# Optimization experiments

Hardware: AMD Instinct MI355X
Metric: run time of the kernel (lower is better)

## Reference

```python
import jax, jax.numpy as jnp
import numpy as np

B, L, LO, H, V = 8, 1024, 1024, 768, 4096
NUM_TAGS = 256


def _merge_one(tags):
    """Replicates merge_weights() for one sequence of tags [L].

    A maximal run of equal, non-(-1) tags becomes one output row that averages
    the hidden states over the run. A run is only emitted when it is *closed*
    by a tag change or a -1 (so a run ending at the last position is dropped,
    exactly like the torch loop). Remaining rows are zero with bias -100.
    """
    Ls = tags.shape[0]
    pos = jnp.arange(Ls)
    valid = tags != -1
    prev = jnp.concatenate([jnp.full((1,), -2, tags.dtype), tags[:-1]])
    start = valid & ((pos == 0) | (tags != prev) | (prev == -1))
    seg_id = jnp.cumsum(start.astype(jnp.int32)) - 1          # run index per position
    total_runs = seg_id[-1] + 1
    emitted = total_runs - valid[-1].astype(jnp.int32)        # trailing open run dropped
    seg_clip = jnp.clip(seg_id, 0, Ls - 1)
    # run lengths via segment sum (invalid positions contribute 0)
    counts = jax.ops.segment_sum(valid.astype(jnp.float32), seg_clip, num_segments=Ls)
    w = jnp.where(valid & (seg_id >= 0) & (seg_id < emitted),
                  1.0 / jnp.maximum(counts[seg_clip], 1.0), 0.0)
    merge = jnp.zeros((Ls, Ls), jnp.float32).at[seg_clip, pos].add(w)  # [rows, tokens]
    bias = jnp.where(pos < emitted, 0.0, -100.0)
    return merge, bias


def setup_inputs() -> dict:
    key = jax.random.key(0)
    k1, k2, k3, k4 = jax.random.split(key, 4)
    hidden1_states = jax.random.normal(k1, (B, L, H), jnp.float32)
    hidden2_states = jax.random.normal(k2, (B, LO, H), jnp.float32)
    lm_logits = jax.random.normal(k3, (B, LO, V), jnp.float32)
    tags = jnp.sort(jax.random.randint(k4, (B, L), 0, NUM_TAGS), axis=-1)
    return {"hidden1_states": hidden1_states, "hidden2_states": hidden2_states,
            "lm_logits": lm_logits, "tags": tags}


def reference(hidden1_states, hidden2_states, lm_logits, tags):
    merge, bias = jax.vmap(_merge_one)(tags)                     # [B,L,L], [B,L]
    attn = jnp.einsum('bls,bsh->blh', merge, hidden1_states)     # segment means
    attn1 = jnp.einsum('boh,blh->bol', hidden2_states, attn) + bias[:, None, :]
    return jnp.concatenate([lm_logits, attn1], axis=2)           # [B,LO,V+L]
```

## Files before the change

### kernel.cpp

```cpp
#include <hip/hip_runtime.h>
#include <hip/hip_bf16.h>
#include <stdint.h>

#define BB   8
#define LL   1024
#define LOO  1024
#define HH   768
#define VV   4096
#define OUTW 5120
#define EMAX 256

typedef unsigned short ushort_t;
typedef __attribute__((ext_vector_type(4))) float   f32x4;
typedef __attribute__((ext_vector_type(8))) __bf16  bf16x8;
typedef __attribute__((ext_vector_type(4))) float   float4v;
typedef __attribute__((ext_vector_type(4))) int     int4v;
typedef __attribute__((ext_vector_type(4))) unsigned short ushort4v;

static __device__ __forceinline__ ushort_t f2bf(float f) {
    union { float f; uint32_t u; } v; v.f = f;
    uint32_t u = v.u;
    uint32_t r = (u + 0x7fffu + ((u >> 16) & 1u)) >> 16;
    return (ushort_t)r;
}

__global__ __launch_bounds__(256) void attn_fused_kernel(
        const float* __restrict__ h1,
        const int* __restrict__ tags,
        ushort_t* __restrict__ attn,
        int* __restrict__ emitted_out) {
    int b = blockIdx.x >> 8;
    int r = blockIdx.x & 255;
    int tid = threadIdx.x;

    __shared__ int stags[LL];
    __shared__ int cnt[256];
    __shared__ int runpos[EMAX + 2];

    ((int4v*)stags)[tid] = ((const int4v*)(tags + b * LL))[tid];
    __syncthreads();

    int p0 = tid * 4;
    int st[4];
    int prevm1 = (p0 == 0) ? -2 : stags[p0 - 1];
    st[0] = (p0 == 0) || (stags[p0] != prevm1);
    st[1] = (stags[p0 + 1] != stags[p0]);
    st[2] = (stags[p0 + 2] != stags[p0 + 1]);
    st[3] = (stags[p0 + 3] != stags[p0 + 2]);
    int c = st[0] + st[1] + st[2] + st[3];
    cnt[tid] = c;
    __syncthreads();
    for (int off = 1; off < 256; off <<= 1) {
        int v = cnt[tid];
        int a = (tid >= off) ? cnt[tid - off] : 0;
        __syncthreads();
        cnt[tid] = v + a;
        __syncthreads();
    }
    int total = cnt[255];
    int base = cnt[tid] - c;
#pragma unroll
    for (int j = 0; j < 4; ++j)
        if (st[j]) runpos[base++] = p0 + j;
    if (tid == 0) runpos[total] = LL;
    __syncthreads();

    int em = total - 1;
    if (r == 0 && tid == 0) emitted_out[b] = em;

    ushort_t* arow = attn + ((size_t)b * EMAX + r) * HH;
    if (r >= em) {
        arow[tid] = 0; arow[tid + 256] = 0; arow[tid + 512] = 0;
        return;
    }
    int s = runpos[r], e = runpos[r + 1];
    float inv = 1.0f / (float)(e - s);
    const float* hb = h1 + (size_t)b * LL * HH;
    float a0 = 0.f, a1 = 0.f, a2 = 0.f;
    for (int p = s; p < e; ++p) {
        const float* row = hb + (size_t)p * HH;
        a0 += row[tid]; a1 += row[tid + 256]; a2 += row[tid + 512];
    }
    arow[tid]       = f2bf(a0 * inv);
    arow[tid + 256] = f2bf(a1 * inv);
    arow[tid + 512] = f2bf(a2 * inv);
}

__global__ __launch_bounds__(256, 4) void fused_out_kernel(
        const float* __restrict__ h2,
        const ushort_t* __restrict__ Bm,
        const int* __restrict__ emitted,
        const float* __restrict__ lm,
        float* __restrict__ out) {
    __shared__ char smem[34816];

    const int bid = blockIdx.x;
    const int b   = bid >> 6;
    const int r0  = (bid & 63) << 4;

    const int tid  = threadIdx.x;
    const int lane = tid & 63;
    const int w    = tid >> 6;

    const float*    Ab = h2 + ((size_t)b * LOO + r0) * HH;
    const ushort_t* Bb = Bm + (size_t)b * EMAX * HH;

    f32x4 zero = {0.f, 0.f, 0.f, 0.f};
    f32x4 acc[4];
    acc[0] = zero; acc[1] = zero; acc[2] = zero; acc[3] = zero;

    const int arow_s = tid >> 4;
    const int akq    = tid & 15;
    for (int k0 = 0; k0 < HH; k0 += 64) {
        __syncthreads();
        {
            f32x4 v = *(const f32x4*)(Ab + (size_t)arow_s * HH + k0 + akq * 4);
            ushort4v o;
            o[0] = f2bf(v[0]); o[1] = f2bf(v[1]); o[2] = f2bf(v[2]); o[3] = f2bf(v[3]);
            *(ushort4v*)(smem + arow_s * 128 + ((akq * 8) ^ ((arow_s & 7) << 4))) = o;
        }
#pragma unroll
        for (int i = 0; i < 8; ++i) {
            int off = i * 4096 + tid * 16;
            int row = off >> 7;
            int cb  = off & 127;
            int scb = cb ^ ((row & 7) << 4);
            const ushort_t* gb = Bb + (size_t)row * HH + k0 + (scb >> 1);
            __builtin_amdgcn_global_load_lds(
                (const __attribute__((address_space(1))) void*)gb,
                (__attribute__((address_space(3))) void*)(smem + 2048 + off), 16, 0, 0);
        }
        asm volatile("s_waitcnt vmcnt(0)" ::: "memory");
        __syncthreads();

#pragma unroll
        for (int ks = 0; ks < 2; ++ks) {
            int kb   = (ks << 6) + ((lane >> 4) << 4);
            int ar   = lane & 15;
            bf16x8 af = *(const bf16x8*)(smem + ar * 128 + (kb ^ ((ar & 7) << 4)));
#pragma unroll
            for (int ni = 0; ni < 4; ++ni) {
                int br = ((w << 2) + ni) * 16 + (lane & 15);
                bf16x8 bf = *(const bf16x8*)(smem + 2048 + br * 128 + (kb ^ ((br & 7) << 4)));
                acc[ni] = __builtin_amdgcn_mfma_f32_16x16x32_bf16(af, bf, acc[ni], 0, 0, 0);
            }
        }
    }

    {
        int em = emitted[b];
        float* outb = out + ((size_t)b * LOO + r0) * OUTW + VV;
#pragma unroll
        for (int ni = 0; ni < 4; ++ni) {
            int l = ((w << 2) + ni) * 16 + (lane & 15);
            float badd = (l < em) ? 0.0f : -100.0f;
            int rbase = (lane >> 4) << 2;
#pragma unroll
            for (int rr = 0; rr < 4; ++rr)
                outb[(size_t)(rbase + rr) * OUTW + l] = acc[ni][rr] + badd;
        }
    }

    const float4v* lm4 = (const float4v*)lm + ((size_t)b * LOO + r0) * (VV / 4);
    float4v* o4 = (float4v*)out + ((size_t)b * LOO + r0) * (OUTW / 4);
    float4v fv = {-100.f, -100.f, -100.f, -100.f};
#pragma unroll 2
    for (int r = 0; r < 16; ++r) {
        float4v v0 = __builtin_nontemporal_load(&lm4[r * 1024 + tid]);
        float4v v1 = __builtin_nontemporal_load(&lm4[r * 1024 + tid + 256]);
        float4v v2 = __builtin_nontemporal_load(&lm4[r * 1024 + tid + 512]);
        float4v v3 = __builtin_nontemporal_load(&lm4[r * 1024 + tid + 768]);
        __builtin_nontemporal_store(v0, &o4[r * 1280 + tid]);
        __builtin_nontemporal_store(v1, &o4[r * 1280 + tid + 256]);
        __builtin_nontemporal_store(v2, &o4[r * 1280 + tid + 512]);
        __builtin_nontemporal_store(v3, &o4[r * 1280 + tid + 768]);
        if (tid < 192)
            __builtin_nontemporal_store(fv, &o4[r * 1280 + 1088 + tid]);
    }
}

extern "C" void kernel_launch(void* const* d_in, const int* in_sizes, int n_in,
                              void* d_out, int out_size, void* d_ws, size_t ws_size,
                              hipStream_t stream) {
    const float* h1   = (const float*)d_in[0];
    const float* h2   = (const float*)d_in[1];
    const float* lm   = (const float*)d_in[2];
    const int*   tags = (const int*)d_in[3];
    float* out = (float*)d_out;

    char* ws = (char*)d_ws;
    ushort_t* attn    = (ushort_t*)ws;
    int*      emitted = (int*)(ws + 3145728);

    attn_fused_kernel<<<BB * EMAX, 256, 0, stream>>>(h1, tags, attn, emitted);
    fused_out_kernel<<<512, 256, 0, stream>>>(h2, attn, emitted, lm, out);
}
```

Measured before the change: 86.32 us.

## Restructure segment-mean into position-chunk blocks and split GEMM from logits copy

The segment-mean kernel now assigns each block a 64-position chunk and a 256-column slice, locating the runs in that chunk by binary search and striding over columns per thread, so h1 is read more contiguously by fewer blocks. The output kernel is split into 64 larger GEMM blocks (128x256 tiles, 512 threads, register-prefetched double staging with padded LDS rows) and 1024 separate copy blocks for the lm_logits passthrough and the -100 fill. This aims to improve B-operand reuse and let the memory-bound copy run alongside the GEMM. The trade-off is that only 64 GEMM blocks exist, which may underuse the CUs, and the padded-stride LDS layout may introduce bank conflicts.

```diff
diff --git a/kernel.cpp b/kernel.cpp
--- a/kernel.cpp
+++ b/kernel.cpp
@@ -13,9 +13,9 @@
 typedef unsigned short ushort_t;
 typedef __attribute__((ext_vector_type(4))) float   f32x4;
 typedef __attribute__((ext_vector_type(8))) __bf16  bf16x8;
+typedef __attribute__((ext_vector_type(4))) __bf16  bf16x4;
 typedef __attribute__((ext_vector_type(4))) float   float4v;
 typedef __attribute__((ext_vector_type(4))) int     int4v;
-typedef __attribute__((ext_vector_type(4))) unsigned short ushort4v;
 
 static __device__ __forceinline__ ushort_t f2bf(float f) {
     union { float f; uint32_t u; } v; v.f = f;
@@ -24,18 +24,19 @@
     return (ushort_t)r;
 }
 
-__global__ __launch_bounds__(256) void attn_fused_kernel(
+__global__ __launch_bounds__(256) void attn_stream_kernel(
         const float* __restrict__ h1,
         const int* __restrict__ tags,
         ushort_t* __restrict__ attn,
         int* __restrict__ emitted_out) {
-    int b = blockIdx.x >> 8;
-    int r = blockIdx.x & 255;
-    int tid = threadIdx.x;
+    const int rc  = blockIdx.x;
+    const int cc  = blockIdx.y;
+    const int b   = blockIdx.z;
+    const int tid = threadIdx.x;
 
     __shared__ int stags[LL];
     __shared__ int cnt[256];
-    __shared__ int runpos[EMAX + 2];
+    __shared__ int runpos[EMAX + 1];
 
     ((int4v*)stags)[tid] = ((const int4v*)(tags + b * LL))[tid];
     __syncthreads();
@@ -47,8 +48,8 @@
     st[1] = (stags[p0 + 1] != stags[p0]);
     st[2] = (stags[p0 + 2] != stags[p0 + 1]);
     st[3] = (stags[p0 + 3] != stags[p0 + 2]);
-    int c = st[0] + st[1] + st[2] + st[3];
-    cnt[tid] = c;
+    int c4 = st[0] + st[1] + st[2] + st[3];
+    cnt[tid] = c4;
     __syncthreads();
     for (int off = 1; off < 256; off <<= 1) {
         int v = cnt[tid];
@@ -58,7 +59,7 @@
         __syncthreads();
     }
     int total = cnt[255];
-    int base = cnt[tid] - c;
+    int base = cnt[tid] - c4;
 #pragma unroll
     for (int j = 0; j < 4; ++j)
         if (st[j]) runpos[base++] = p0 + j;
@@ -66,116 +67,147 @@
     __syncthreads();
 
     int em = total - 1;
-    if (r == 0 && tid == 0) emitted_out[b] = em;
-
-    ushort_t* arow = attn + ((size_t)b * EMAX + r) * HH;
-    if (r >= em) {
-        arow[tid] = 0; arow[tid + 256] = 0; arow[tid + 512] = 0;
-        return;
-    }
-    int s = runpos[r], e = runpos[r + 1];
-    float inv = 1.0f / (float)(e - s);
-    const float* hb = h1 + (size_t)b * LL * HH;
-    float a0 = 0.f, a1 = 0.f, a2 = 0.f;
-    for (int p = s; p < e; ++p) {
-        const float* row = hb + (size_t)p * HH;
-        a0 += row[tid]; a1 += row[tid + 256]; a2 += row[tid + 512];
-    }
-    arow[tid]       = f2bf(a0 * inv);
-    arow[tid + 256] = f2bf(a1 * inv);
-    arow[tid + 512] = f2bf(a2 * inv);
-}
-
-__global__ __launch_bounds__(256, 4) void fused_out_kernel(
+    if (rc == 0 && cc == 0 && tid == 0) emitted_out[b] = em;
+
+    const int rlo = rc << 6, rhi = rlo + 64;
+    int lo;
+    { int a = 0, z = total;
+      while (a < z) { int m = (a + z) >> 1; if (runpos[m] < rlo) a = m + 1; else z = m; }
+      lo = a; }
+    int hi;
+    { int a = lo, z = total;
+      while (a < z) { int m = (a + z) >> 1; if (runpos[m] < rhi) a = m + 1; else z = m; }
+      hi = a; }
+    int send = hi < em ? hi : em;
+
+    const int c = (cc << 8) + tid;
+    const float* hb = h1 + (size_t)b * LL * HH + c;
+    for (int s = lo; s < send; ++s) {
+        int ps = runpos[s], pe = runpos[s + 1];
+        float acc = 0.f;
+        for (int p = ps; p < pe; ++p) acc += hb[(size_t)p * HH];
+        attn[((size_t)b * EMAX + s) * HH + c] = f2bf(acc / (float)(pe - ps));
+    }
+    if (rc == 15) {
+        for (int r = em; r < EMAX; ++r)
+            attn[((size_t)b * EMAX + r) * HH + c] = 0;
+    }
+}
+
+#define NGEMM 64
+__global__ __launch_bounds__(512, 4) void mega2_kernel(
         const float* __restrict__ h2,
         const ushort_t* __restrict__ Bm,
         const int* __restrict__ emitted,
         const float* __restrict__ lm,
         float* __restrict__ out) {
-    __shared__ char smem[34816];
+    __shared__ char smem[30720];
 
     const int bid = blockIdx.x;
-    const int b   = bid >> 6;
-    const int r0  = (bid & 63) << 4;
-
-    const int tid  = threadIdx.x;
+    const int tid = threadIdx.x;
+
+    if (bid >= NGEMM) {
+        int cid = bid - NGEMM;
+        const float4v* lm4 = (const float4v*)lm + (size_t)cid * 8 * 1024;
+        float4v* o4 = (float4v*)out + (size_t)cid * 8 * 1280;
+        const float4v fv = {-100.f, -100.f, -100.f, -100.f};
+#pragma unroll
+        for (int r = 0; r < 8; r += 2) {
+            float4v v0 = __builtin_nontemporal_load(&lm4[(size_t)(r    ) * 1024 + tid]);
+            float4v v1 = __builtin_nontemporal_load(&lm4[(size_t)(r    ) * 1024 + tid + 512]);
+            float4v v2 = __builtin_nontemporal_load(&lm4[(size_t)(r + 1) * 1024 + tid]);
+            float4v v3 = __builtin_nontemporal_load(&lm4[(size_t)(r + 1) * 1024 + tid + 512]);
+            __builtin_nontemporal_store(v0, &o4[(size_t)(r    ) * 1280 + tid]);
+            __builtin_nontemporal_store(v1, &o4[(size_t)(r    ) * 1280 + tid + 512]);
+            __builtin_nontemporal_store(v2, &o4[(size_t)(r + 1) * 1280 + tid]);
+            __builtin_nontemporal_store(v3, &o4[(size_t)(r + 1) * 1280 + tid + 512]);
+            if (tid < 192) {
+                __builtin_nontemporal_store(fv, &o4[(size_t)(r    ) * 1280 + 1088 + tid]);
+                __builtin_nontemporal_store(fv, &o4[(size_t)(r + 1) * 1280 + 1088 + tid]);
+            }
+        }
+        return;
+    }
+
+    const int b  = bid >> 3;
+    const int rt = bid & 7;
+    const int R0 = rt << 7;
     const int lane = tid & 63;
-    const int w    = tid >> 6;
-
-    const float*    Ab = h2 + ((size_t)b * LOO + r0) * HH;
+    const int wid  = tid >> 6;
+    const int wr   = wid >> 1;
+    const int wc   = wid & 1;
+
+    const float*    Ab = h2 + ((size_t)b * LOO + R0) * HH;
     const ushort_t* Bb = Bm + (size_t)b * EMAX * HH;
 
-    f32x4 zero = {0.f, 0.f, 0.f, 0.f};
-    f32x4 acc[4];
-    acc[0] = zero; acc[1] = zero; acc[2] = zero; acc[3] = zero;
-
-    const int arow_s = tid >> 4;
-    const int akq    = tid & 15;
-    for (int k0 = 0; k0 < HH; k0 += 64) {
+    char* As = smem;
+    char* Bs = smem + 10240;
+
+    const int ar0 = tid >> 3,          aq0 = tid & 7;
+    const int ar1 = (tid + 512) >> 3,  aq1 = tid & 7;
+    const int br0 = tid >> 2,          bs0 = tid & 3;
+    const int br1 = (tid + 512) >> 2,  bs1 = tid & 3;
+
+    f32x4  aR0, aR1;
+    bf16x8 bR0, bR1;
+    f32x4 acc0[8], acc1[8];
+#pragma unroll
+    for (int i = 0; i < 8; ++i) {
+        acc0[i] = (f32x4){0.f, 0.f, 0.f, 0.f};
+        acc1[i] = (f32x4){0.f, 0.f, 0.f, 0.f};
+    }
+
+    aR0 = *(const f32x4*)(Ab + (size_t)ar0 * HH + aq0 * 4);
+    aR1 = *(const f32x4*)(Ab + (size_t)ar1 * HH + aq1 * 4);
+    bR0 = *(const bf16x8*)(Bb + (size_t)br0 * HH + bs0 * 8);
+    bR1 = *(const bf16x8*)(Bb + (size_t)br1 * HH + bs1 * 8);
+
+    for (int ks = 0; ks < 24; ++ks) {
         __syncthreads();
         {
-            f32x4 v = *(const f32x4*)(Ab + (size_t)arow_s * HH + k0 + akq * 4);
-            ushort4v o;
-            o[0] = f2bf(v[0]); o[1] = f2bf(v[1]); o[2] = f2bf(v[2]); o[3] = f2bf(v[3]);
-            *(ushort4v*)(smem + arow_s * 128 + ((akq * 8) ^ ((arow_s & 7) << 4))) = o;
-        }
-#pragma unroll
-        for (int i = 0; i < 8; ++i) {
-            int off = i * 4096 + tid * 16;
-            int row = off >> 7;
-            int cb  = off & 127;
-            int scb = cb ^ ((row & 7) << 4);
-            const ushort_t* gb = Bb + (size_t)row * HH + k0 + (scb >> 1);
-            __builtin_amdgcn_global_load_lds(
-                (const __attribute__((address_space(1))) void*)gb,
-                (__attribute__((address_space(3))) void*)(smem + 2048 + off), 16, 0, 0);
-        }
-        asm volatile("s_waitcnt vmcnt(0)" ::: "memory");
-        __syncthreads();
-
-#pragma unroll
-        for (int ks = 0; ks < 2; ++ks) {
-            int kb   = (ks << 6) + ((lane >> 4) << 4);
-            int ar   = lane & 15;
-            bf16x8 af = *(const bf16x8*)(smem + ar * 128 + (kb ^ ((ar & 7) << 4)));
-#pragma unroll
-            for (int ni = 0; ni < 4; ++ni) {
-                int br = ((w << 2) + ni) * 16 + (lane & 15);
-                bf16x8 bf = *(const bf16x8*)(smem + 2048 + br * 128 + (kb ^ ((br & 7) << 4)));
-                acc[ni] = __builtin_amdgcn_mfma_f32_16x16x32_bf16(af, bf, acc[ni], 0, 0, 0);
+            bf16x4 t0, t1;
+            t0[0] = (__bf16)aR0[0]; t0[1] = (__bf16)aR0[1];
+            t0[2] = (__bf16)aR0[2]; t0[3] = (__bf16)aR0[3];
+            t1[0] = (__bf16)aR1[0]; t1[1] = (__bf16)aR1[1];
+            t1[2] = (__bf16)aR1[2]; t1[3] = (__bf16)aR1[3];
+            *(bf16x4*)(As + ar0 * 80 + aq0 * 8) = t0;
+            *(bf16x4*)(As + ar1 * 80 + aq1 * 8) = t1;
+            *(bf16x8*)(Bs + br0 * 80 + bs0 * 16) = bR0;
+            *(bf16x8*)(Bs + br1 * 80 + bs1 * 16) = bR1;
+        }
+        __syncthreads();
+        if (ks < 23) {
+            int k0 = (ks + 1) << 5;
+            aR0 = *(const f32x4*)(Ab + (size_t)ar0 * HH + k0 + aq0 * 4);
+            aR1 = *(const f32x4*)(Ab + (size_t)ar1 * HH + k0 + aq1 * 4);
+            bR0 = *(const bf16x8*)(Bb + (size_t)br0 * HH + k0 + bs0 * 8);
+            bR1 = *(const bf16x8*)(Bb + (size_t)br1 * HH + k0 + bs1 * 8);
+        }
+        {
+            const int hb16 = (lane >> 4) << 4;
+            bf16x8 af0 = *(const bf16x8*)(As + (wr * 32 +  0 + (lane & 15)) * 80 + hb16);
+            bf16x8 af1 = *(const bf16x8*)(As + (wr * 32 + 16 + (lane & 15)) * 80 + hb16);
+#pragma unroll
+            for (int ni = 0; ni < 8; ++ni) {
+                bf16x8 bfv = *(const bf16x8*)(Bs + (wc * 128 + ni * 16 + (lane & 15)) * 80 + hb16);
+                acc0[ni] = __builtin_amdgcn_mfma_f32_16x16x32_bf16(af0, bfv, acc0[ni], 0, 0, 0);
+                acc1[ni] = __builtin_amdgcn_mfma_f32_16x16x32_bf16(af1, bfv, acc1[ni], 0, 0, 0);
             }
         }
     }
 
-    {
-        int em = emitted[b];
-        float* outb = out + ((size_t)b * LOO + r0) * OUTW + VV;
-#pragma unroll
-        for (int ni = 0; ni < 4; ++ni) {
-            int l = ((w << 2) + ni) * 16 + (lane & 15);
-            float badd = (l < em) ? 0.0f : -100.0f;
-            int rbase = (lane >> 4) << 2;
-#pragma unroll
-            for (int rr = 0; rr < 4; ++rr)
-                outb[(size_t)(rbase + rr) * OUTW + l] = acc[ni][rr] + badd;
-        }
-    }
-
-    const float4v* lm4 = (const float4v*)lm + ((size_t)b * LOO + r0) * (VV / 4);
-    float4v* o4 = (float4v*)out + ((size_t)b * LOO + r0) * (OUTW / 4);
-    float4v fv = {-100.f, -100.f, -100.f, -100.f};
-#pragma unroll 2
-    for (int r = 0; r < 16; ++r) {
-        float4v v0 = __builtin_nontemporal_load(&lm4[r * 1024 + tid]);
-        float4v v1 = __builtin_nontemporal_load(&lm4[r * 1024 + tid + 256]);
-        float4v v2 = __builtin_nontemporal_load(&lm4[r * 1024 + tid + 512]);
-        float4v v3 = __builtin_nontemporal_load(&lm4[r * 1024 + tid + 768]);
-        __builtin_nontemporal_store(v0, &o4[r * 1280 + tid]);
-        __builtin_nontemporal_store(v1, &o4[r * 1280 + tid + 256]);
-        __builtin_nontemporal_store(v2, &o4[r * 1280 + tid + 512]);
-        __builtin_nontemporal_store(v3, &o4[r * 1280 + tid + 768]);
-        if (tid < 192)
-            __builtin_nontemporal_store(fv, &o4[r * 1280 + 1088 + tid]);
+    const int em = emitted[b];
+    float* outb = out + ((size_t)b * LOO + R0) * OUTW + VV;
+    const int rb = wr * 32 + ((lane >> 4) << 2);
+#pragma unroll
+    for (int ni = 0; ni < 8; ++ni) {
+        int l = wc * 128 + ni * 16 + (lane & 15);
+        float badd = (l < em) ? 0.0f : -100.0f;
+#pragma unroll
+        for (int rr = 0; rr < 4; ++rr) {
+            outb[(size_t)(rb + rr) * OUTW + l]      = acc0[ni][rr] + badd;
+            outb[(size_t)(rb + 16 + rr) * OUTW + l] = acc1[ni][rr] + badd;
+        }
     }
 }
 
@@ -192,6 +224,6 @@
     ushort_t* attn    = (ushort_t*)ws;
     int*      emitted = (int*)(ws + 3145728);
 
-    attn_fused_kernel<<<BB * EMAX, 256, 0, stream>>>(h1, tags, attn, emitted);
-    fused_out_kernel<<<512, 256, 0, stream>>>(h2, attn, emitted, lm, out);
-}
+    attn_stream_kernel<<<dim3(16, 3, 8), 256, 0, stream>>>(h1, tags, attn, emitted);
+    mega2_kernel<<<NGEMM + 1024, 512, 0, stream>>>(h2, attn, emitted, lm, out);
+}
```

Result: slower. 89.04 us (+3.2%).
